# Performance work log

Measured on AMD Instinct MI355X. Metric: run time of the kernel, lower is better.

Reference implementation:

```python
import jax, jax.numpy as jnp
import numpy as np

D = 1024      # dim_input
H = 16        # n_heads
DH = 64       # dim_inner
S = 1024      # current_seq
M = 1024      # pre_seq (memory)
B = 2         # batch
SCALE = 1.0 / np.sqrt(DH)


def _rel_shift(x):
    # x: [S, J, B, H]; Transformer-XL relative shift
    s, j = x.shape[0], x.shape[1]
    zero = jnp.zeros((s, 1) + x.shape[2:], x.dtype)
    x = jnp.concatenate([zero, x], axis=1)            # [S, J+1, B, H]
    x = x.reshape((j + 1, s) + x.shape[2:])[1:]        # [J, S, B, H]
    return x.reshape((s, j) + x.shape[2:])             # [S, J, B, H]


def setup_inputs() -> dict:
    key = jax.random.key(0)
    ks = jax.random.split(key, 9)
    std = 1.0 / np.sqrt(D)
    return {
        "multi_head_input": jax.random.normal(ks[0], (S, B, D), jnp.float32),
        "position_emb": jax.random.normal(ks[1], (S + M, D), jnp.float32),
        "memory": jax.random.normal(ks[2], (M, B, D), jnp.float32),
        "u": jax.random.normal(ks[3], (H, DH), jnp.float32) * 0.02,
        "v": jax.random.normal(ks[4], (H, DH), jnp.float32) * 0.02,
        "W_kv": jax.random.normal(ks[5], (D, 2 * H * DH), jnp.float32) * std,
        "W_q": jax.random.normal(ks[6], (D, H * DH), jnp.float32) * std,
        "W_pos": jax.random.normal(ks[7], (D, H * DH), jnp.float32) * std,
        "W_out": jax.random.normal(ks[8], (H * DH, D), jnp.float32) * std,
    }


def reference(multi_head_input, position_emb, memory, u, v, W_kv, W_q, W_pos, W_out):
    s = multi_head_input.shape[0]
    m = memory.shape[0]
    b = multi_head_input.shape[1]
    x_mem = jnp.concatenate([memory, multi_head_input], axis=0)   # [M+S, B, D]
    kv = x_mem @ W_kv                                              # [M+S, B, 2*H*DH]
    k, val = jnp.split(kv, 2, axis=-1)
    k = k.reshape(m + s, b, H, DH)
    val = val.reshape(m + s, b, H, DH)
    q = (multi_head_input @ W_q).reshape(s, b, H, DH)              # [S, B, H, DH]

    # content term: (q + u) . k
    content = jnp.einsum('ibhd,jbhd->ijbh', q + u, k)              # [S, M+S, B, H]
    # position term: (q + v) . r, then rel_shift
    r = (position_emb @ W_pos).reshape(m + s, H, DH)               # [M+S, H, DH]
    pos = jnp.einsum('ibhd,jhd->ijbh', q + v, r)                   # [S, M+S, B, H]
    pos = _rel_shift(pos)

    attn = jax.nn.softmax((content + pos) * SCALE, axis=1)         # [S, M+S, B, H]
    out = jnp.einsum('ijbh,jbhd->ibhd', attn, val).reshape(s, b, H * DH)
    return out @ W_out                                             # [S, B, D]
```

## Files before the change

kernel.cpp:

```cpp
#include <hip/hip_runtime.h>
#include <hip/hip_bf16.h>
#include <hip/hip_fp16.h>
#include <math.h>

#define D    1024
#define H    16
#define DH   64
#define S    1024
#define M    1024
#define B    2
#define J    2048
#define SCALE 0.125f

typedef __attribute__((ext_vector_type(8))) short        bf16x8;
typedef __attribute__((ext_vector_type(4))) short        s16x4;
typedef __attribute__((ext_vector_type(8))) _Float16     h16x8;
typedef __attribute__((ext_vector_type(8))) unsigned short us8;
typedef __attribute__((ext_vector_type(4))) float        f32x4;

__device__ __forceinline__ unsigned short f2bf(float f) {
    __hip_bfloat16 t = __float2bfloat16(f);
    unsigned short r; __builtin_memcpy(&r, &t, 2); return r;
}
__device__ __forceinline__ short f2bs(float f) {
    __hip_bfloat16 t = __float2bfloat16(f);
    short r; __builtin_memcpy(&r, &t, 2); return r;
}

__device__ __forceinline__ void g2l16(const short* g, short* l) {
    __builtin_amdgcn_global_load_lds(
        (const __attribute__((address_space(1))) unsigned int*)g,
        (__attribute__((address_space(3))) unsigned int*)l, 16, 0, 0);
}

__global__ __launch_bounds__(256)
void prep(const float* __restrict__ mem, const float* __restrict__ x,
          const float* __restrict__ pemb,
          const float* __restrict__ Wkv, const float* __restrict__ Wq,
          const float* __restrict__ Wpos, const float* __restrict__ Wout,
          short* __restrict__ a_bf, short* __restrict__ p_bf,
          short* __restrict__ wkvt, short* __restrict__ wqt,
          short* __restrict__ wpt,  short* __restrict__ wot)
{
    __shared__ float t[64][65];
    int blk = blockIdx.x;
    const int tid = threadIdx.x;
    if (blk < 6144) {
        const int idx = (blk * 256 + tid) * 4;
        const int TWO_M = 2 * 1024 * 1024;
        float4 v; short* dst;
        if (idx < TWO_M)          { v = *(const float4*)(mem  + idx);           dst = a_bf + idx; }
        else if (idx < 2 * TWO_M) { v = *(const float4*)(x    + idx - TWO_M);   dst = a_bf + idx; }
        else                      { v = *(const float4*)(pemb + idx - 2*TWO_M); dst = p_bf + idx - 2*TWO_M; }
        s16x4 o = { f2bs(v.x), f2bs(v.y), f2bs(v.z), f2bs(v.w) };
        *(s16x4*)dst = o;
        return;
    }
    blk -= 6144;
    const float* src; short* dst; int N, t0;
    if (blk < 512)       { src = Wkv;  dst = wkvt; N = 2048; t0 = blk; }
    else if (blk < 768)  { src = Wq;   dst = wqt;  N = 1024; t0 = blk - 512; }
    else if (blk < 1024) { src = Wpos; dst = wpt;  N = 1024; t0 = blk - 768; }
    else                 { src = Wout; dst = wot;  N = 1024; t0 = blk - 1024; }
    const int ntn = N >> 6;
    const int k0 = (t0 / ntn) * 64, n0 = (t0 % ntn) * 64;
    #pragma unroll
    for (int e = tid; e < 4096; e += 256) {
        int r = e >> 6, c = e & 63;
        t[r][c] = src[(size_t)(k0 + r) * N + n0 + c];
    }
    __syncthreads();
    #pragma unroll
    for (int e = tid; e < 4096; e += 256) {
        int nr = e >> 6, kc = e & 63;
        dst[(size_t)(n0 + nr) * 1024 + k0 + kc] = f2bs(t[kc][nr]);
    }
}

__device__ __forceinline__ void gemm_core(const short* __restrict__ A,
                                          const short* __restrict__ Bt,
                                          short* As, short* Bs,
                                          int bm0, int bn0, int tid,
                                          f32x4 acc[4][4])
{
    const int w    = tid >> 6;
    const int wy   = w >> 1, wx = w & 1;
    const int lane = tid & 63;
    const int lm   = lane & 15;
    const int lq   = lane >> 4;

    for (int k0 = 0; k0 < 1024; k0 += 64) {
        const short* Ab = A  + (size_t)bm0 * 1024 + k0;
        const short* Bb = Bt + (size_t)bn0 * 1024 + k0;
        #pragma unroll
        for (int t = 0; t < 4; ++t) {
            int s = t * 256 + tid;
            int r = s >> 3, c = s & 7;
            int cg = c ^ (r & 7);
            g2l16(Ab + r * 1024 + cg * 8, As + s * 8);
            g2l16(Bb + r * 1024 + cg * 8, Bs + s * 8);
        }
        __syncthreads();
        #pragma unroll
        for (int kk = 0; kk < 2; ++kk) {
            bf16x8 af[4], bg[4];
            #pragma unroll
            for (int r4 = 0; r4 < 4; ++r4) {
                int ar = wy * 64 + r4 * 16 + lm;
                int kc = kk * 4 + lq;
                af[r4] = *(const bf16x8*)(As + ((ar << 3) + (kc ^ (ar & 7))) * 8);
            }
            #pragma unroll
            for (int c4 = 0; c4 < 4; ++c4) {
                int br = wx * 64 + c4 * 16 + lm;
                int kc = kk * 4 + lq;
                bg[c4] = *(const bf16x8*)(Bs + ((br << 3) + (kc ^ (br & 7))) * 8);
            }
            #pragma unroll
            for (int r4 = 0; r4 < 4; ++r4)
                #pragma unroll
                for (int c4 = 0; c4 < 4; ++c4)
                    acc[r4][c4] = __builtin_amdgcn_mfma_f32_16x16x32_bf16(
                        af[r4], bg[c4], acc[r4][c4], 0, 0, 0);
        }
        __syncthreads();
    }
}

__global__ __launch_bounds__(256)
void proj_fused(const short* __restrict__ a_bf, const short* __restrict__ p_bf,
                const short* __restrict__ wkvt, const short* __restrict__ wqt,
                const short* __restrict__ wpt,
                short* __restrict__ k_bf, short* __restrict__ vt_bf,
                short* __restrict__ qu_bf, short* __restrict__ qv_bf,
                short* __restrict__ r_bf,
                const float* __restrict__ uvec, const float* __restrict__ vvec)
{
    __shared__ __align__(16) short As[128 * 64];
    __shared__ __align__(16) short Bs[128 * 64];

    int blk = blockIdx.x;
    int mode, bx, by;
    const short *A, *Bt;
    if (blk < 512)      { bx = blk & 15; by = blk >> 4;
                          if (bx >= 8) { mode = 4; A = wkvt; Bt = a_bf; }
                          else         { mode = 0; A = a_bf; Bt = wkvt; } }
    else if (blk < 640) { int b2 = blk - 512; mode = 1; bx = b2 & 7; by = b2 >> 3;
                          A = a_bf + (size_t)2048 * 1024; Bt = wqt; }
    else                { int b3 = blk - 640; mode = 2; bx = b3 & 7; by = b3 >> 3;
                          A = p_bf; Bt = wpt; }
    const int bn0 = (mode == 4) ? by * 128 : bx * 128;
    const int bm0 = (mode == 4) ? bx * 128 : by * 128;
    const int tid = threadIdx.x;
    const int w = tid >> 6, wy = w >> 1, wx = w & 1;
    const int lane = tid & 63, lm = lane & 15, lq = lane >> 4;

    f32x4 acc[4][4];
    #pragma unroll
    for (int r = 0; r < 4; ++r)
        #pragma unroll
        for (int c = 0; c < 4; ++c) acc[r][c] = (f32x4){0.f, 0.f, 0.f, 0.f};

    gemm_core(A, Bt, As, Bs, bm0, bn0, tid, acc);

    #pragma unroll
    for (int r4 = 0; r4 < 4; ++r4) {
        #pragma unroll
        for (int c4 = 0; c4 < 4; ++c4) {
            const int n = bn0 + wx * 64 + c4 * 16 + lm;
            float ubias = 0.f, vbias = 0.f;
            if (mode == 1) { ubias = uvec[n]; vbias = vvec[n]; }
            #pragma unroll
            for (int reg = 0; reg < 4; ++reg) {
                const int m = bm0 + wy * 64 + r4 * 16 + lq * 4 + reg;
                const float val = acc[r4][c4][reg];
                if (mode == 0) {
                    int j = m >> 1, b = m & 1;
                    int h = n >> 6, d = n & 63;
                    k_bf[(((size_t)b * H + h) * J + j) * DH + d] = f2bs(val);
                } else if (mode == 4) {
                    int n2 = m - 1024, h = n2 >> 6, d = n2 & 63;
                    int j = n >> 1, b = n & 1;
                    vt_bf[(((size_t)b * H + h) * DH + d) * J + j] = f2bs(val);
                } else if (mode == 1) {
                    int i = m >> 1, b = m & 1;
                    int h = n >> 6, d = n & 63;
                    size_t o = (((size_t)b * H + h) * S + i) * DH + d;
                    qu_bf[o] = f2bs((val + ubias) * SCALE);
                    qv_bf[o] = f2bs((val + vbias) * SCALE);
                } else {
                    int h = n >> 6, d = n & 63;
                    r_bf[((size_t)h * J + m) * DH + d] = f2bs(val);
                }
            }
        }
    }
}

__global__ __launch_bounds__(256)
void gemm_out(const short* __restrict__ A, const short* __restrict__ Bt,
              float* __restrict__ out)
{
    __shared__ __align__(16) short As[128 * 64];
    __shared__ __align__(16) short Bs[128 * 64];
    const int bn0 = blockIdx.x * 128, bm0 = blockIdx.y * 128;
    const int tid = threadIdx.x;
    const int w = tid >> 6, wy = w >> 1, wx = w & 1;
    const int lane = tid & 63, lm = lane & 15, lq = lane >> 4;

    f32x4 acc[4][4];
    #pragma unroll
    for (int r = 0; r < 4; ++r)
        #pragma unroll
        for (int c = 0; c < 4; ++c) acc[r][c] = (f32x4){0.f, 0.f, 0.f, 0.f};

    gemm_core(A, Bt, As, Bs, bm0, bn0, tid, acc);

    #pragma unroll
    for (int r4 = 0; r4 < 4; ++r4)
        #pragma unroll
        for (int c4 = 0; c4 < 4; ++c4) {
            const int n = bn0 + wx * 64 + c4 * 16 + lm;
            #pragma unroll
            for (int reg = 0; reg < 4; ++reg) {
                const int m = bm0 + wy * 64 + r4 * 16 + lq * 4 + reg;
                out[(size_t)m * 1024 + n] = acc[r4][c4][reg];
            }
        }
}

__device__ __forceinline__ int sidx(int m, int c) {
    return (m << 10) + (c ^ (m << 3));
}

__global__ __launch_bounds__(512)
void attn_mfma(const short* __restrict__ qu_bf, const short* __restrict__ qv_bf,
               const short* __restrict__ k_bf,  const short* __restrict__ vt_bf,
               const short* __restrict__ r_bf,
               float* __restrict__ opart, float* __restrict__ ml)
{
    __shared__ unsigned short sc[32 * 1024];
    __half* sch = (__half*)sc;
    float*  scF = (float*)sc;

    const int bh  = blockIdx.x;
    const int it  = blockIdx.y;
    const int jh  = blockIdx.z;
    const int i0  = it * 32;
    const int cbeg = jh << 10, cend = cbeg + 1024;
    const int h   = bh & (H - 1);
    const int tid = threadIdx.x;
    const int w    = tid >> 6;
    const int lane = tid & 63;
    const int lm   = lane & 15;
    const int lq   = lane >> 4;
    const int slot = (it * 32 + bh) * 2 + jh;

    const short* qup0 = qu_bf + ((size_t)(bh * S + i0 + lm)) * DH + lq * 8;
    const short* qup1 = qup0 + 16 * DH;
    bf16x8 au00 = *(const bf16x8*)qup0,        au01 = *(const bf16x8*)(qup0 + 32);
    bf16x8 au10 = *(const bf16x8*)qup1,        au11 = *(const bf16x8*)(qup1 + 32);
    const short* qvp0 = qv_bf + ((size_t)(bh * S + i0 + lm)) * DH + lq * 8;
    const short* qvp1 = qvp0 + 16 * DH;
    bf16x8 av00 = *(const bf16x8*)qvp0,        av01 = *(const bf16x8*)(qvp0 + 32);
    bf16x8 av10 = *(const bf16x8*)qvp1,        av11 = *(const bf16x8*)(qvp1 + 32);
    int r1a = i0 + 1 + lm;  if (r1a > S - 1) r1a = S - 1;
    int r1b = i0 + 17 + lm; if (r1b > S - 1) r1b = S - 1;
    const short* qwp0 = qv_bf + ((size_t)(bh * S + r1a)) * DH + lq * 8;
    const short* qwp1 = qv_bf + ((size_t)(bh * S + r1b)) * DH + lq * 8;
    bf16x8 aw00 = *(const bf16x8*)qwp0,        aw01 = *(const bf16x8*)(qwp0 + 32);
    bf16x8 aw10 = *(const bf16x8*)qwp1,        aw11 = *(const bf16x8*)(qwp1 + 32);

    if (tid < 32) {
        int hole = i0 + tid + 1025;
        if (hole >= cbeg && hole < cend) sc[sidx(tid, hole - cbeg)] = 0;
    }

    const short* rbase = r_bf + (size_t)h * J * DH;

    {
        int tmp = cbeg + 977 - i0;
        int tlo = tmp > 0 ? ((tmp + 15) >> 4) : 0;
        int thi = (cend + 1022 - i0) >> 4; if (thi > 127) thi = 127;
        for (int t = tlo + w; t <= thi; t += 8) {
            const short* rp = rbase + (size_t)(t * 16 + lm) * DH + lq * 8;
            bf16x8 b0 = *(const bf16x8*)rp;
            bf16x8 b1 = *(const bf16x8*)(rp + 32);
            f32x4 c0 = {0.f,0.f,0.f,0.f}, c1 = {0.f,0.f,0.f,0.f};
            c0 = __builtin_amdgcn_mfma_f32_16x16x32_bf16(av00, b0, c0, 0, 0, 0);
            c1 = __builtin_amdgcn_mfma_f32_16x16x32_bf16(av10, b0, c1, 0, 0, 0);
            c0 = __builtin_amdgcn_mfma_f32_16x16x32_bf16(av01, b1, c0, 0, 0, 0);
            c1 = __builtin_amdgcn_mfma_f32_16x16x32_bf16(av11, b1, c1, 0, 0, 0);
            int cb = i0 + t * 16 + lm - 1023;
            #pragma unroll
            for (int r = 0; r < 4; ++r) {
                int m0 = lq * 4 + r, m1 = m0 + 16;
                int col0 = cb + m0, col1 = cb + m1;
                if (col0 >= cbeg && col0 < cend)
                    sch[sidx(m0, col0 - cbeg)] = __float2half(c0[r]);
                if (col1 >= cbeg && col1 < cend)
                    sch[sidx(m1, col1 - cbeg)] = __float2half(c1[r]);
            }
        }
    }

    {
        int tmpw = cbeg - 1072 - i0;
        int tlw = tmpw > 0 ? ((tmpw + 15) >> 4) : 0;
        int thw = (cend - 1027 - i0) >> 4; if (thw > 127) thw = 127;
        for (int t = tlw + w; t <= thw; t += 8) {
            const short* rp = rbase + (size_t)(t * 16 + lm) * DH + lq * 8;
            bf16x8 b0 = *(const bf16x8*)rp;
            bf16x8 b1 = *(const bf16x8*)(rp + 32);
            f32x4 c0 = {0.f,0.f,0.f,0.f}, c1 = {0.f,0.f,0.f,0.f};
            c0 = __builtin_amdgcn_mfma_f32_16x16x32_bf16(aw00, b0, c0, 0, 0, 0);
            c1 = __builtin_amdgcn_mfma_f32_16x16x32_bf16(aw10, b0, c1, 0, 0, 0);
            c0 = __builtin_amdgcn_mfma_f32_16x16x32_bf16(aw01, b1, c0, 0, 0, 0);
            c1 = __builtin_amdgcn_mfma_f32_16x16x32_bf16(aw11, b1, c1, 0, 0, 0);
            int cb = i0 + t * 16 + lm + 1026;
            #pragma unroll
            for (int r = 0; r < 4; ++r) {
                int m0 = lq * 4 + r, m1 = m0 + 16;
                int col0 = cb + m0, col1 = cb + m1;
                if (col0 >= cbeg && col0 < cend)
                    sch[sidx(m0, col0 - cbeg)] = __float2half(c0[r]);
                if (col1 >= cbeg && col1 < cend)
                    sch[sidx(m1, col1 - cbeg)] = __float2half(c1[r]);
            }
        }
    }
    __syncthreads();

    const short* kbase = k_bf + (size_t)bh * J * DH;
    for (int g = 0; g < 8; ++g) {
        int t = jh * 64 + w + 8 * ((g + it) & 7);
        const short* kp = kbase + (size_t)(t * 16 + lm) * DH + lq * 8;
        bf16x8 b0 = *(const bf16x8*)kp;
        bf16x8 b1 = *(const bf16x8*)(kp + 32);
        int lc = t * 16 + lm - cbeg;
        f32x4 c0, c1;
        #pragma unroll
        for (int r = 0; r < 4; ++r) {
            c0[r] = __half2float(sch[sidx(lq * 4 + r, lc)]);
            c1[r] = __half2float(sch[sidx(16 + lq * 4 + r, lc)]);
        }
        c0 = __builtin_amdgcn_mfma_f32_16x16x32_bf16(au00, b0, c0, 0, 0, 0);
        c1 = __builtin_amdgcn_mfma_f32_16x16x32_bf16(au10, b0, c1, 0, 0, 0);
        c0 = __builtin_amdgcn_mfma_f32_16x16x32_bf16(au01, b1, c0, 0, 0, 0);
        c1 = __builtin_amdgcn_mfma_f32_16x16x32_bf16(au11, b1, c1, 0, 0, 0);
        #pragma unroll
        for (int r = 0; r < 4; ++r) {
            sch[sidx(lq * 4 + r, lc)]      = __float2half(c0[r]);
            sch[sidx(16 + lq * 4 + r, lc)] = __float2half(c1[r]);
        }
    }
    __syncthreads();

    {
        const int row = tid >> 4;
        const int cw  = (tid & 15) * 8;
        float mx = -1e30f;
        #pragma unroll
        for (int c = cw; c < 1024; c += 128) {
            h16x8 v = *(const h16x8*)(sc + sidx(row, c));
            #pragma unroll
            for (int k = 0; k < 8; ++k) mx = fmaxf(mx, (float)v[k]);
        }
        #pragma unroll
        for (int off = 1; off < 16; off <<= 1) mx = fmaxf(mx, __shfl_xor(mx, off));
        float ssum = 0.f;
        #pragma unroll
        for (int c = cw; c < 1024; c += 128) {
            int idx = sidx(row, c);
            h16x8 v = *(const h16x8*)(sc + idx);
            us8 e;
            #pragma unroll
            for (int k = 0; k < 8; ++k) {
                float ex = __expf((float)v[k] - mx);
                ssum += ex;
                e[k] = f2bf(ex);
            }
            *(us8*)(sc + idx) = e;
        }
        #pragma unroll
        for (int off = 1; off < 16; off <<= 1) ssum += __shfl_xor(ssum, off);
        if ((tid & 15) == 0) {
            ml[(size_t)slot * 64 + row * 2]     = mx;
            ml[(size_t)slot * 64 + row * 2 + 1] = ssum;
        }
    }
    __syncthreads();

    const int dslice = w & 3, jq = w >> 2;
    const short* vtb = vt_bf + ((size_t)bh * DH + dslice * 16 + lm) * J + cbeg + jq * 512;
    f32x4 pa0 = {0.f,0.f,0.f,0.f}, pa1 = {0.f,0.f,0.f,0.f};
    f32x4 pa2 = {0.f,0.f,0.f,0.f}, pa3 = {0.f,0.f,0.f,0.f};
    f32x4 pb0 = {0.f,0.f,0.f,0.f}, pb1 = {0.f,0.f,0.f,0.f};
    f32x4 pb2 = {0.f,0.f,0.f,0.f}, pb3 = {0.f,0.f,0.f,0.f};
    #pragma unroll 1
    for (int jo0 = 0; jo0 < 4; ++jo0) {
        int j0 = ((jo0 + it) & 3) * 128;
        bf16x8 bv0 = *(const bf16x8*)(vtb + j0 +  0 + lq * 8);
        bf16x8 bv1 = *(const bf16x8*)(vtb + j0 + 32 + lq * 8);
        bf16x8 bv2 = *(const bf16x8*)(vtb + j0 + 64 + lq * 8);
        bf16x8 bv3 = *(const bf16x8*)(vtb + j0 + 96 + lq * 8);
        int lb = jq * 512 + j0;
        bf16x8 a0 = *(const bf16x8*)(sc + sidx(lm, lb +  0 + lq * 8));
        bf16x8 a1 = *(const bf16x8*)(sc + sidx(lm, lb + 32 + lq * 8));
        bf16x8 a2 = *(const bf16x8*)(sc + sidx(lm, lb + 64 + lq * 8));
        bf16x8 a3 = *(const bf16x8*)(sc + sidx(lm, lb + 96 + lq * 8));
        bf16x8 c0 = *(const bf16x8*)(sc + sidx(16 + lm, lb +  0 + lq * 8));
        bf16x8 c1 = *(const bf16x8*)(sc + sidx(16 + lm, lb + 32 + lq * 8));
        bf16x8 c2 = *(const bf16x8*)(sc + sidx(16 + lm, lb + 64 + lq * 8));
        bf16x8 c3 = *(const bf16x8*)(sc + sidx(16 + lm, lb + 96 + lq * 8));
        pa0 = __builtin_amdgcn_mfma_f32_16x16x32_bf16(a0, bv0, pa0, 0, 0, 0);
        pb0 = __builtin_amdgcn_mfma_f32_16x16x32_bf16(c0, bv0, pb0, 0, 0, 0);
        pa1 = __builtin_amdgcn_mfma_f32_16x16x32_bf16(a1, bv1, pa1, 0, 0, 0);
        pb1 = __builtin_amdgcn_mfma_f32_16x16x32_bf16(c1, bv1, pb1, 0, 0, 0);
        pa2 = __builtin_amdgcn_mfma_f32_16x16x32_bf16(a2, bv2, pa2, 0, 0, 0);
        pb2 = __builtin_amdgcn_mfma_f32_16x16x32_bf16(c2, bv2, pb2, 0, 0, 0);
        pa3 = __builtin_amdgcn_mfma_f32_16x16x32_bf16(a3, bv3, pa3, 0, 0, 0);
        pb3 = __builtin_amdgcn_mfma_f32_16x16x32_bf16(c3, bv3, pb3, 0, 0, 0);
    }
    __syncthreads();

    #pragma unroll
    for (int r = 0; r < 4; ++r) {
        int m0 = lq * 4 + r, m1 = m0 + 16;
        scF[jq * 2048 + m0 * 64 + dslice * 16 + lm] = pa0[r] + pa1[r] + pa2[r] + pa3[r];
        scF[jq * 2048 + m1 * 64 + dslice * 16 + lm] = pb0[r] + pb1[r] + pb2[r] + pb3[r];
    }
    __syncthreads();

    float* op = opart + (size_t)slot * 2048;
    #pragma unroll
    for (int e = tid; e < 2048; e += 512)
        op[e] = scF[e] + scF[2048 + e];
}

__global__ __launch_bounds__(256)
void attn_combine(const float* __restrict__ opart, const float* __restrict__ ml,
                  short* __restrict__ o_bf)
{
    const int blk = blockIdx.x;
    const int it = blk >> 5, bh = blk & 31;
    const int h = bh & 15, b = bh >> 4;
    __shared__ float wgt[32][2];
    const int tid = threadIdx.x;
    if (tid < 32) {
        float m0 = ml[(size_t)(blk * 2 + 0) * 64 + tid * 2];
        float l0 = ml[(size_t)(blk * 2 + 0) * 64 + tid * 2 + 1];
        float m1 = ml[(size_t)(blk * 2 + 1) * 64 + tid * 2];
        float l1 = ml[(size_t)(blk * 2 + 1) * 64 + tid * 2 + 1];
        float mx = fmaxf(m0, m1);
        float e0 = __expf(m0 - mx), e1 = __expf(m1 - mx);
        float inv = 1.0f / (e0 * l0 + e1 * l1);
        wgt[tid][0] = e0 * inv;
        wgt[tid][1] = e1 * inv;
    }
    __syncthreads();
    const float* p0 = opart + (size_t)(blk * 2 + 0) * 2048;
    const float* p1 = opart + (size_t)(blk * 2 + 1) * 2048;
    #pragma unroll
    for (int e = tid; e < 2048; e += 256) {
        int m = e >> 6, d = e & 63;
        float val = p0[e] * wgt[m][0] + p1[e] * wgt[m][1];
        o_bf[((size_t)(it * 32 + m) * B + b) * (H * DH) + h * DH + d] = f2bs(val);
    }
}

extern "C" void kernel_launch(void* const* d_in, const int* in_sizes, int n_in,
                              void* d_out, int out_size, void* d_ws, size_t ws_size,
                              hipStream_t stream)
{
    const float* x    = (const float*)d_in[0];
    const float* pemb = (const float*)d_in[1];
    const float* mem  = (const float*)d_in[2];
    const float* u    = (const float*)d_in[3];
    const float* v    = (const float*)d_in[4];
    const float* Wkv  = (const float*)d_in[5];
    const float* Wq   = (const float*)d_in[6];
    const float* Wpos = (const float*)d_in[7];
    const float* Wout = (const float*)d_in[8];
    float* out = (float*)d_out;

    char* p = (char*)d_ws;
    short* a_bf  = (short*)p; p += (size_t)4096 * 1024 * 2;
    short* p_bf  = (short*)p; p += (size_t)2048 * 1024 * 2;
    short* wkvt  = (short*)p; p += (size_t)2048 * 1024 * 2;
    short* wqt   = (short*)p; p += (size_t)1024 * 1024 * 2;
    short* wpt   = (short*)p; p += (size_t)1024 * 1024 * 2;
    short* wot   = (short*)p; p += (size_t)1024 * 1024 * 2;
    short* k_bf  = (short*)p; p += (size_t)B * H * J * DH * 2;
    short* vt_bf = (short*)p; p += (size_t)B * H * J * DH * 2;
    short* qu_bf = (short*)p; p += (size_t)B * H * S * DH * 2;
    short* qv_bf = (short*)p; p += (size_t)B * H * S * DH * 2;
    short* r_bf  = (short*)p; p += (size_t)H * J * DH * 2;
    short* o_bf  = (short*)p;

    float* opart = (float*)d_ws;
    float* ml    = (float*)((char*)d_ws + (size_t)16 * 1024 * 1024);

    prep<<<7424, 256, 0, stream>>>(mem, x, pemb, Wkv, Wq, Wpos, Wout,
                                   a_bf, p_bf, wkvt, wqt, wpt, wot);
    proj_fused<<<768, 256, 0, stream>>>(a_bf, p_bf, wkvt, wqt, wpt,
                                        k_bf, vt_bf, qu_bf, qv_bf, r_bf, u, v);
    attn_mfma<<<dim3(B * H, S / 32, 2), 512, 0, stream>>>(
        qu_bf, qv_bf, k_bf, vt_bf, r_bf, opart, ml);
    attn_combine<<<(S / 32) * B * H, 256, 0, stream>>>(opart, ml, o_bf);
    gemm_out<<<dim3(8, 16), 256, 0, stream>>>(o_bf, wot, out);
}
```

Measured before the change: 301.4 us.

## Prefetch K/V tiles across barriers, unroll pos loop, cheaper softmax max/exp

After: 297.5 us. Within noise of the previous version (-1.3%).

```diff
diff --git a/kernel.cpp b/kernel.cpp
--- a/kernel.cpp
+++ b/kernel.cpp
@@ -15,6 +15,7 @@
 typedef __attribute__((ext_vector_type(8))) short        bf16x8;
 typedef __attribute__((ext_vector_type(4))) short        s16x4;
 typedef __attribute__((ext_vector_type(8))) _Float16     h16x8;
+typedef __attribute__((ext_vector_type(2))) _Float16     h2;
 typedef __attribute__((ext_vector_type(8))) unsigned short us8;
 typedef __attribute__((ext_vector_type(4))) float        f32x4;
 
@@ -25,6 +26,10 @@
 __device__ __forceinline__ short f2bs(float f) {
     __hip_bfloat16 t = __float2bfloat16(f);
     short r; __builtin_memcpy(&r, &t, 2); return r;
+}
+__device__ __forceinline__ unsigned short f2bf_fast(float f) {
+    unsigned int u; __builtin_memcpy(&u, &f, 4);
+    return (unsigned short)((u + 0x8000u) >> 16);
 }
 
 __device__ __forceinline__ void g2l16(const short* g, short* l) {
@@ -282,10 +287,37 @@
         int tmp = cbeg + 977 - i0;
         int tlo = tmp > 0 ? ((tmp + 15) >> 4) : 0;
         int thi = (cend + 1022 - i0) >> 4; if (thi > 127) thi = 127;
-        for (int t = tlo + w; t <= thi; t += 8) {
+        int t = tlo + w;
+        for (; t + 8 <= thi; t += 16) {
+            const short* rp0 = rbase + (size_t)(t * 16 + lm) * DH + lq * 8;
+            const short* rp1 = rbase + (size_t)((t + 8) * 16 + lm) * DH + lq * 8;
+            bf16x8 b0 = *(const bf16x8*)rp0, b1 = *(const bf16x8*)(rp0 + 32);
+            bf16x8 b2 = *(const bf16x8*)rp1, b3 = *(const bf16x8*)(rp1 + 32);
+            f32x4 c0 = {0.f,0.f,0.f,0.f}, c1 = {0.f,0.f,0.f,0.f};
+            f32x4 c2 = {0.f,0.f,0.f,0.f}, c3 = {0.f,0.f,0.f,0.f};
+            c0 = __builtin_amdgcn_mfma_f32_16x16x32_bf16(av00, b0, c0, 0, 0, 0);
+            c1 = __builtin_amdgcn_mfma_f32_16x16x32_bf16(av10, b0, c1, 0, 0, 0);
+            c2 = __builtin_amdgcn_mfma_f32_16x16x32_bf16(av00, b2, c2, 0, 0, 0);
+            c3 = __builtin_amdgcn_mfma_f32_16x16x32_bf16(av10, b2, c3, 0, 0, 0);
+            c0 = __builtin_amdgcn_mfma_f32_16x16x32_bf16(av01, b1, c0, 0, 0, 0);
+            c1 = __builtin_amdgcn_mfma_f32_16x16x32_bf16(av11, b1, c1, 0, 0, 0);
+            c2 = __builtin_amdgcn_mfma_f32_16x16x32_bf16(av01, b3, c2, 0, 0, 0);
+            c3 = __builtin_amdgcn_mfma_f32_16x16x32_bf16(av11, b3, c3, 0, 0, 0);
+            int cb0 = i0 + t * 16 + lm - 1023;
+            int cb1 = cb0 + 128;
+            #pragma unroll
+            for (int r = 0; r < 4; ++r) {
+                int m0 = lq * 4 + r, m1 = m0 + 16;
+                int cA = cb0 + m0, cB = cb0 + m1, cC = cb1 + m0, cD = cb1 + m1;
+                if (cA >= cbeg && cA < cend) sch[sidx(m0, cA - cbeg)] = __float2half(c0[r]);
+                if (cB >= cbeg && cB < cend) sch[sidx(m1, cB - cbeg)] = __float2half(c1[r]);
+                if (cC >= cbeg && cC < cend) sch[sidx(m0, cC - cbeg)] = __float2half(c2[r]);
+                if (cD >= cbeg && cD < cend) sch[sidx(m1, cD - cbeg)] = __float2half(c3[r]);
+            }
+        }
+        if (t <= thi) {
             const short* rp = rbase + (size_t)(t * 16 + lm) * DH + lq * 8;
-            bf16x8 b0 = *(const bf16x8*)rp;
-            bf16x8 b1 = *(const bf16x8*)(rp + 32);
+            bf16x8 b0 = *(const bf16x8*)rp, b1 = *(const bf16x8*)(rp + 32);
             f32x4 c0 = {0.f,0.f,0.f,0.f}, c1 = {0.f,0.f,0.f,0.f};
             c0 = __builtin_amdgcn_mfma_f32_16x16x32_bf16(av00, b0, c0, 0, 0, 0);
             c1 = __builtin_amdgcn_mfma_f32_16x16x32_bf16(av10, b0, c1, 0, 0, 0);
@@ -295,11 +327,9 @@
             #pragma unroll
             for (int r = 0; r < 4; ++r) {
                 int m0 = lq * 4 + r, m1 = m0 + 16;
-                int col0 = cb + m0, col1 = cb + m1;
-                if (col0 >= cbeg && col0 < cend)
-                    sch[sidx(m0, col0 - cbeg)] = __float2half(c0[r]);
-                if (col1 >= cbeg && col1 < cend)
-                    sch[sidx(m1, col1 - cbeg)] = __float2half(c1[r]);
+                int cA = cb + m0, cB = cb + m1;
+                if (cA >= cbeg && cA < cend) sch[sidx(m0, cA - cbeg)] = __float2half(c0[r]);
+                if (cB >= cbeg && cB < cend) sch[sidx(m1, cB - cbeg)] = __float2half(c1[r]);
             }
         }
     }
@@ -310,8 +340,7 @@
         int thw = (cend - 1027 - i0) >> 4; if (thw > 127) thw = 127;
         for (int t = tlw + w; t <= thw; t += 8) {
             const short* rp = rbase + (size_t)(t * 16 + lm) * DH + lq * 8;
-            bf16x8 b0 = *(const bf16x8*)rp;
-            bf16x8 b1 = *(const bf16x8*)(rp + 32);
+            bf16x8 b0 = *(const bf16x8*)rp, b1 = *(const bf16x8*)(rp + 32);
             f32x4 c0 = {0.f,0.f,0.f,0.f}, c1 = {0.f,0.f,0.f,0.f};
             c0 = __builtin_amdgcn_mfma_f32_16x16x32_bf16(aw00, b0, c0, 0, 0, 0);
             c1 = __builtin_amdgcn_mfma_f32_16x16x32_bf16(aw10, b0, c1, 0, 0, 0);
@@ -321,53 +350,92 @@
             #pragma unroll
             for (int r = 0; r < 4; ++r) {
                 int m0 = lq * 4 + r, m1 = m0 + 16;
-                int col0 = cb + m0, col1 = cb + m1;
-                if (col0 >= cbeg && col0 < cend)
-                    sch[sidx(m0, col0 - cbeg)] = __float2half(c0[r]);
-                if (col1 >= cbeg && col1 < cend)
-                    sch[sidx(m1, col1 - cbeg)] = __float2half(c1[r]);
-            }
-        }
-    }
-    __syncthreads();
+                int cA = cb + m0, cB = cb + m1;
+                if (cA >= cbeg && cA < cend) sch[sidx(m0, cA - cbeg)] = __float2half(c0[r]);
+                if (cB >= cbeg && cB < cend) sch[sidx(m1, cB - cbeg)] = __float2half(c1[r]);
+            }
+        }
+    }
 
     const short* kbase = k_bf + (size_t)bh * J * DH;
-    for (int g = 0; g < 8; ++g) {
-        int t = jh * 64 + w + 8 * ((g + it) & 7);
-        const short* kp = kbase + (size_t)(t * 16 + lm) * DH + lq * 8;
-        bf16x8 b0 = *(const bf16x8*)kp;
-        bf16x8 b1 = *(const bf16x8*)(kp + 32);
-        int lc = t * 16 + lm - cbeg;
-        f32x4 c0, c1;
+    int tc0 = jh * 64 + w + 8 * ((it) & 7);
+    int tc1 = jh * 64 + w + 8 * ((1 + it) & 7);
+    const short* kp0 = kbase + (size_t)(tc0 * 16 + lm) * DH + lq * 8;
+    const short* kp1 = kbase + (size_t)(tc1 * 16 + lm) * DH + lq * 8;
+    bf16x8 kb0 = *(const bf16x8*)kp0, kb1 = *(const bf16x8*)(kp0 + 32);
+    bf16x8 kb2 = *(const bf16x8*)kp1, kb3 = *(const bf16x8*)(kp1 + 32);
+    __syncthreads();
+
+    #pragma unroll 1
+    for (int g = 0; g < 8; g += 2) {
+        int t0 = jh * 64 + w + 8 * ((g + it) & 7);
+        int t1 = jh * 64 + w + 8 * ((g + 1 + it) & 7);
+        bf16x8 nb0, nb1, nb2, nb3;
+        if (g + 2 < 8) {
+            int u0 = jh * 64 + w + 8 * ((g + 2 + it) & 7);
+            int u1 = jh * 64 + w + 8 * ((g + 3 + it) & 7);
+            const short* np0 = kbase + (size_t)(u0 * 16 + lm) * DH + lq * 8;
+            const short* np1 = kbase + (size_t)(u1 * 16 + lm) * DH + lq * 8;
+            nb0 = *(const bf16x8*)np0; nb1 = *(const bf16x8*)(np0 + 32);
+            nb2 = *(const bf16x8*)np1; nb3 = *(const bf16x8*)(np1 + 32);
+        }
+        int lc0 = t0 * 16 + lm - cbeg;
+        int lc1 = t1 * 16 + lm - cbeg;
+        f32x4 c0, c1, c2, c3;
         #pragma unroll
         for (int r = 0; r < 4; ++r) {
-            c0[r] = __half2float(sch[sidx(lq * 4 + r, lc)]);
-            c1[r] = __half2float(sch[sidx(16 + lq * 4 + r, lc)]);
-        }
-        c0 = __builtin_amdgcn_mfma_f32_16x16x32_bf16(au00, b0, c0, 0, 0, 0);
-        c1 = __builtin_amdgcn_mfma_f32_16x16x32_bf16(au10, b0, c1, 0, 0, 0);
-        c0 = __builtin_amdgcn_mfma_f32_16x16x32_bf16(au01, b1, c0, 0, 0, 0);
-        c1 = __builtin_amdgcn_mfma_f32_16x16x32_bf16(au11, b1, c1, 0, 0, 0);
+            c0[r] = __half2float(sch[sidx(lq * 4 + r, lc0)]);
+            c1[r] = __half2float(sch[sidx(16 + lq * 4 + r, lc0)]);
+            c2[r] = __half2float(sch[sidx(lq * 4 + r, lc1)]);
+            c3[r] = __half2float(sch[sidx(16 + lq * 4 + r, lc1)]);
+        }
+        c0 = __builtin_amdgcn_mfma_f32_16x16x32_bf16(au00, kb0, c0, 0, 0, 0);
+        c1 = __builtin_amdgcn_mfma_f32_16x16x32_bf16(au10, kb0, c1, 0, 0, 0);
+        c2 = __builtin_amdgcn_mfma_f32_16x16x32_bf16(au00, kb2, c2, 0, 0, 0);
+        c3 = __builtin_amdgcn_mfma_f32_16x16x32_bf16(au10, kb2, c3, 0, 0, 0);
+        c0 = __builtin_amdgcn_mfma_f32_16x16x32_bf16(au01, kb1, c0, 0, 0, 0);
+        c1 = __builtin_amdgcn_mfma_f32_16x16x32_bf16(au11, kb1, c1, 0, 0, 0);
+        c2 = __builtin_amdgcn_mfma_f32_16x16x32_bf16(au01, kb3, c2, 0, 0, 0);
+        c3 = __builtin_amdgcn_mfma_f32_16x16x32_bf16(au11, kb3, c3, 0, 0, 0);
         #pragma unroll
         for (int r = 0; r < 4; ++r) {
-            sch[sidx(lq * 4 + r, lc)]      = __float2half(c0[r]);
-            sch[sidx(16 + lq * 4 + r, lc)] = __float2half(c1[r]);
-        }
+            sch[sidx(lq * 4 + r, lc0)]      = __float2half(c0[r]);
+            sch[sidx(16 + lq * 4 + r, lc0)] = __float2half(c1[r]);
+            sch[sidx(lq * 4 + r, lc1)]      = __float2half(c2[r]);
+            sch[sidx(16 + lq * 4 + r, lc1)] = __float2half(c3[r]);
+        }
+        kb0 = nb0; kb1 = nb1; kb2 = nb2; kb3 = nb3;
+    }
+
+    const int dslice = w & 3, jq = w >> 2;
+    const short* vtb = vt_bf + ((size_t)bh * DH + dslice * 16 + lm) * J + cbeg + jq * 512;
+    bf16x8 cv0, cv1, cv2, cv3;
+    {
+        int j0 = (it & 3) * 128;
+        cv0 = *(const bf16x8*)(vtb + j0 +  0 + lq * 8);
+        cv1 = *(const bf16x8*)(vtb + j0 + 32 + lq * 8);
+        cv2 = *(const bf16x8*)(vtb + j0 + 64 + lq * 8);
+        cv3 = *(const bf16x8*)(vtb + j0 + 96 + lq * 8);
     }
     __syncthreads();
 
     {
         const int row = tid >> 4;
         const int cw  = (tid & 15) * 8;
-        float mx = -1e30f;
+        h2 pm = { (_Float16)(-60000.0f), (_Float16)(-60000.0f) };
         #pragma unroll
         for (int c = cw; c < 1024; c += 128) {
             h16x8 v = *(const h16x8*)(sc + sidx(row, c));
-            #pragma unroll
-            for (int k = 0; k < 8; ++k) mx = fmaxf(mx, (float)v[k]);
-        }
+            h2* vp = (h2*)&v;
+            pm = __builtin_elementwise_max(pm,
+                     __builtin_elementwise_max(
+                         __builtin_elementwise_max(vp[0], vp[1]),
+                         __builtin_elementwise_max(vp[2], vp[3])));
+        }
+        float mx = fmaxf((float)pm[0], (float)pm[1]);
         #pragma unroll
         for (int off = 1; off < 16; off <<= 1) mx = fmaxf(mx, __shfl_xor(mx, off));
+        const float mx14 = mx * 1.44269504f;
         float ssum = 0.f;
         #pragma unroll
         for (int c = cw; c < 1024; c += 128) {
@@ -376,9 +444,9 @@
             us8 e;
             #pragma unroll
             for (int k = 0; k < 8; ++k) {
-                float ex = __expf((float)v[k] - mx);
+                float ex = __builtin_amdgcn_exp2f((float)v[k] * 1.44269504f - mx14);
                 ssum += ex;
-                e[k] = f2bf(ex);
+                e[k] = f2bf_fast(ex);
             }
             *(us8*)(sc + idx) = e;
         }
@@ -391,19 +459,21 @@
     }
     __syncthreads();
 
-    const int dslice = w & 3, jq = w >> 2;
-    const short* vtb = vt_bf + ((size_t)bh * DH + dslice * 16 + lm) * J + cbeg + jq * 512;
     f32x4 pa0 = {0.f,0.f,0.f,0.f}, pa1 = {0.f,0.f,0.f,0.f};
     f32x4 pa2 = {0.f,0.f,0.f,0.f}, pa3 = {0.f,0.f,0.f,0.f};
     f32x4 pb0 = {0.f,0.f,0.f,0.f}, pb1 = {0.f,0.f,0.f,0.f};
     f32x4 pb2 = {0.f,0.f,0.f,0.f}, pb3 = {0.f,0.f,0.f,0.f};
     #pragma unroll 1
     for (int jo0 = 0; jo0 < 4; ++jo0) {
+        bf16x8 nv0, nv1, nv2, nv3;
+        if (jo0 < 3) {
+            int jn = ((jo0 + 1 + it) & 3) * 128;
+            nv0 = *(const bf16x8*)(vtb + jn +  0 + lq * 8);
+            nv1 = *(const bf16x8*)(vtb + jn + 32 + lq * 8);
+            nv2 = *(const bf16x8*)(vtb + jn + 64 + lq * 8);
+            nv3 = *(const bf16x8*)(vtb + jn + 96 + lq * 8);
+        }
         int j0 = ((jo0 + it) & 3) * 128;
-        bf16x8 bv0 = *(const bf16x8*)(vtb + j0 +  0 + lq * 8);
-        bf16x8 bv1 = *(const bf16x8*)(vtb + j0 + 32 + lq * 8);
-        bf16x8 bv2 = *(const bf16x8*)(vtb + j0 + 64 + lq * 8);
-        bf16x8 bv3 = *(const bf16x8*)(vtb + j0 + 96 + lq * 8);
         int lb = jq * 512 + j0;
         bf16x8 a0 = *(const bf16x8*)(sc + sidx(lm, lb +  0 + lq * 8));
         bf16x8 a1 = *(const bf16x8*)(sc + sidx(lm, lb + 32 + lq * 8));
@@ -413,14 +483,15 @@
         bf16x8 c1 = *(const bf16x8*)(sc + sidx(16 + lm, lb + 32 + lq * 8));
         bf16x8 c2 = *(const bf16x8*)(sc + sidx(16 + lm, lb + 64 + lq * 8));
         bf16x8 c3 = *(const bf16x8*)(sc + sidx(16 + lm, lb + 96 + lq * 8));
-        pa0 = __builtin_amdgcn_mfma_f32_16x16x32_bf16(a0, bv0, pa0, 0, 0, 0);
-        pb0 = __builtin_amdgcn_mfma_f32_16x16x32_bf16(c0, bv0, pb0, 0, 0, 0);
-        pa1 = __builtin_amdgcn_mfma_f32_16x16x32_bf16(a1, bv1, pa1, 0, 0, 0);
-        pb1 = __builtin_amdgcn_mfma_f32_16x16x32_bf16(c1, bv1, pb1, 0, 0, 0);
-        pa2 = __builtin_amdgcn_mfma_f32_16x16x32_bf16(a2, bv2, pa2, 0, 0, 0);
-        pb2 = __builtin_amdgcn_mfma_f32_16x16x32_bf16(c2, bv2, pb2, 0, 0, 0);
-        pa3 = __builtin_amdgcn_mfma_f32_16x16x32_bf16(a3, bv3, pa3, 0, 0, 0);
-        pb3 = __builtin_amdgcn_mfma_f32_16x16x32_bf16(c3, bv3, pb3, 0, 0, 0);
+        pa0 = __builtin_amdgcn_mfma_f32_16x16x32_bf16(a0, cv0, pa0, 0, 0, 0);
+        pb0 = __builtin_amdgcn_mfma_f32_16x16x32_bf16(c0, cv0, pb0, 0, 0, 0);
+        pa1 = __builtin_amdgcn_mfma_f32_16x16x32_bf16(a1, cv1, pa1, 0, 0, 0);
+        pb1 = __builtin_amdgcn_mfma_f32_16x16x32_bf16(c1, cv1, pb1, 0, 0, 0);
+        pa2 = __builtin_amdgcn_mfma_f32_16x16x32_bf16(a2, cv2, pa2, 0, 0, 0);
+        pb2 = __builtin_amdgcn_mfma_f32_16x16x32_bf16(c2, cv2, pb2, 0, 0, 0);
+        pa3 = __builtin_amdgcn_mfma_f32_16x16x32_bf16(a3, cv3, pa3, 0, 0, 0);
+        pb3 = __builtin_amdgcn_mfma_f32_16x16x32_bf16(c3, cv3, pb3, 0, 0, 0);
+        if (jo0 < 3) { cv0 = nv0; cv1 = nv1; cv2 = nv2; cv3 = nv3; }
     }
     __syncthreads();
 
```
